# Performance work log

Measured on AMD Instinct MI355X. Metric: run time of the kernel, lower is better.

The kernel has to match this reference:

```python
import jax, jax.numpy as jnp
import numpy as np

D_MODEL = 768
N_HEADS = 12


def setup_inputs() -> dict:
    key = jax.random.key(0)
    ks = jax.random.split(key, 9)
    s = 1.0 / np.sqrt(D_MODEL)
    return {
        "x": jax.random.normal(ks[0], (1, 4096, D_MODEL), dtype=jnp.float32),
        "w_q": jax.random.normal(ks[1], (D_MODEL, D_MODEL), dtype=jnp.float32) * s,
        "b_q": jnp.zeros((D_MODEL,), dtype=jnp.float32),
        "w_k": jax.random.normal(ks[2], (D_MODEL, D_MODEL), dtype=jnp.float32) * s,
        "b_k": jnp.zeros((D_MODEL,), dtype=jnp.float32),
        "w_v": jax.random.normal(ks[3], (D_MODEL, D_MODEL), dtype=jnp.float32) * s,
        "b_v": jnp.zeros((D_MODEL,), dtype=jnp.float32),
        "w_o": jax.random.normal(ks[4], (D_MODEL, D_MODEL), dtype=jnp.float32) * s,
        "b_o": jnp.zeros((D_MODEL,), dtype=jnp.float32),
    }


def reference(x, w_q, b_q, w_k, b_k, w_v, b_v, w_o, b_o):
    b, l, dm = x.shape
    h = N_HEADS
    dk = dm // h
    # projections ([b,l,dm] @ [dm,dm]) then split heads -> [b,h,l,dk]
    def proj(w, bias):
        y = x @ w + bias
        return y.reshape(b, l, h, dk).transpose(0, 2, 1, 3)
    q = proj(w_q, b_q)
    k = proj(w_k, b_k)
    v = proj(w_v, b_v)
    scale = jnp.asarray(dk, x.dtype) ** 0.5
    scores = jnp.einsum("bhqd,bhkd->bhqk", q, k)  # [b,h,l,l]
    causal = jnp.triu(jnp.ones((l, l), dtype=bool), k=1)
    scores = jnp.where(causal, -jnp.inf, scores)
    weights = jax.nn.softmax(scores / scale, axis=-1)
    heads = jnp.einsum("bhqk,bhkd->bhqd", weights, v)  # [b,h,l,dk]
    heads = heads.transpose(0, 2, 1, 3).reshape(b, l, dm)
    return heads @ w_o + b_o
```

## Files before the change

kernel.cpp:

```cpp
#include <hip/hip_runtime.h>

#define L_SEQ 4096
#define DMODEL 768
#define NH 12
#define DK 64

typedef __bf16 bf16;
typedef __bf16 bf16x8 __attribute__((ext_vector_type(8)));
typedef __bf16 bf16x4 __attribute__((ext_vector_type(4)));
typedef float f32x4 __attribute__((ext_vector_type(4)));

#define QSCALE 0.1803368801111204f
#define DEFER_THR 8.0f

__device__ __forceinline__ void gload16(const void* g, void* l) {
    __builtin_amdgcn_global_load_lds(
        (const __attribute__((address_space(1))) unsigned int*)g,
        (__attribute__((address_space(3))) unsigned int*)l, 16, 0, 0);
}

__global__ __launch_bounds__(256) void prep_kernel(
    const float* __restrict__ x,
    const float* __restrict__ w_q, const float* __restrict__ w_k,
    const float* __restrict__ w_v, const float* __restrict__ w_o,
    bf16* __restrict__ xb, bf16* __restrict__ wqt, bf16* __restrict__ wkt,
    bf16* __restrict__ wvt, bf16* __restrict__ wot)
{
    const int bid = blockIdx.x;
    const int t = threadIdx.x;
    if (bid < 576) {
        __shared__ bf16 Ls[64][72];
        const int mat = bid / 144;
        const int tile = bid % 144;
        const int k0 = (tile / 12) * 64;
        const int c0 = (tile % 12) * 64;
        const float* W = mat == 0 ? w_q : mat == 1 ? w_k : mat == 2 ? w_v : w_o;
        bf16* WT = mat == 0 ? wqt : mat == 1 ? wkt : mat == 2 ? wvt : wot;
        #pragma unroll
        for (int p = 0; p < 4; ++p) {
            int id = t + p * 256;
            int r = id >> 4, c4 = id & 15;
            float4 v = *(const float4*)(W + (size_t)(k0 + r) * DMODEL + c0 + c4 * 4);
            bf16x4 b; b[0] = (bf16)v.x; b[1] = (bf16)v.y; b[2] = (bf16)v.z; b[3] = (bf16)v.w;
            *(bf16x4*)&Ls[r][c4 * 4] = b;
        }
        __syncthreads();
        #pragma unroll
        for (int p = 0; p < 2; ++p) {
            int id = t + p * 256;
            int crow = id >> 3, kc = id & 7;
            bf16x8 o;
            #pragma unroll
            for (int e = 0; e < 8; ++e) o[e] = Ls[kc * 8 + e][crow];
            *(bf16x8*)(WT + (size_t)(c0 + crow) * DMODEL + k0 + kc * 8) = o;
        }
    } else {
        const size_t base = (size_t)(bid - 576) * 4096;
        #pragma unroll
        for (int p = 0; p < 4; ++p) {
            size_t idx = base + (size_t)(t + p * 256) * 4;
            float4 v = *(const float4*)(x + idx);
            bf16x4 b; b[0] = (bf16)v.x; b[1] = (bf16)v.y; b[2] = (bf16)v.z; b[3] = (bf16)v.w;
            *(bf16x4*)(xb + idx) = b;
        }
    }
}

__global__ __launch_bounds__(256) void proj_kernel(
    const bf16* __restrict__ xb,
    const bf16* __restrict__ wqt, const bf16* __restrict__ wkt, const bf16* __restrict__ wvt,
    const float* __restrict__ b_q, const float* __restrict__ b_k, const float* __restrict__ b_v,
    bf16* __restrict__ qbuf, bf16* __restrict__ kbuf, bf16* __restrict__ vt)
{
    __shared__ bf16 As[128][72];
    __shared__ bf16 Bs[64][72];
    const int t = threadIdx.x;
    const int w = t >> 6, l = t & 63;
    const int lg = l >> 4, lr = l & 15;

    if (blockIdx.x < 768) {
        const int bn = blockIdx.x % 24;
        const int bm = blockIdx.x / 24;
        const int m0 = bm * 128;
        const int gn0 = bn * 64;
        const int sel = gn0 / DMODEL;
        const int c0 = gn0 % DMODEL;
        const bf16* WT = sel ? wkt : wqt;
        const float* bias = sel ? b_k : b_q;
        const float scale = sel ? 1.0f : QSCALE;

        f32x4 acc[2][4];
        #pragma unroll
        for (int i = 0; i < 2; i++)
            #pragma unroll
            for (int j = 0; j < 4; j++) acc[i][j] = (f32x4){0.f, 0.f, 0.f, 0.f};

        for (int kk = 0; kk < DMODEL; kk += 64) {
            #pragma unroll
            for (int p = 0; p < 4; ++p) {
                int id = t + p * 256;
                int row = id >> 3, ch = id & 7;
                *(bf16x8*)&As[row][ch * 8] =
                    *(const bf16x8*)(xb + (size_t)(m0 + row) * DMODEL + kk + ch * 8);
            }
            #pragma unroll
            for (int p = 0; p < 2; ++p) {
                int id = t + p * 256;
                int n = id >> 3, ch = id & 7;
                *(bf16x8*)&Bs[n][ch * 8] =
                    *(const bf16x8*)(WT + (size_t)(c0 + n) * DMODEL + kk + ch * 8);
            }
            __syncthreads();
            #pragma unroll
            for (int ks = 0; ks < 2; ++ks) {
                bf16x8 a[2], bfr[4];
                #pragma unroll
                for (int i = 0; i < 2; i++) a[i] = *(const bf16x8*)&As[w * 32 + i * 16 + lr][ks * 32 + lg * 8];
                #pragma unroll
                for (int j = 0; j < 4; j++) bfr[j] = *(const bf16x8*)&Bs[j * 16 + lr][ks * 32 + lg * 8];
                #pragma unroll
                for (int i = 0; i < 2; i++)
                    #pragma unroll
                    for (int j = 0; j < 4; j++)
                        acc[i][j] = __builtin_amdgcn_mfma_f32_16x16x32_bf16(a[i], bfr[j], acc[i][j], 0, 0, 0);
            }
            __syncthreads();
        }
        #pragma unroll
        for (int i = 0; i < 2; i++) {
            #pragma unroll
            for (int j = 0; j < 4; j++) {
                int c = c0 + j * 16 + lr;
                int h = c >> 6, d = c & 63;
                float bb = bias[c];
                #pragma unroll
                for (int r = 0; r < 4; r++) {
                    int m = m0 + w * 32 + i * 16 + lg * 4 + r;
                    float v = (acc[i][j][r] + bb) * scale;
                    if (sel == 0) {
                        qbuf[((size_t)h * L_SEQ + m) * DK + d] = (bf16)v;
                    } else {
                        size_t idx = (size_t)h * L_SEQ * DK + (size_t)(m >> 6) * 4096
                                   + (size_t)(m & 63) * 64 + (((d >> 3) ^ (m & 7)) << 3) + (d & 7);
                        kbuf[idx] = (bf16)v;
                    }
                }
            }
        }
    } else {
        const int bid = blockIdx.x - 768;
        const int bc = bid % 12;
        const int bmm = bid / 12;
        const int c0 = bc * 64;
        const int mm0 = bmm * 128;

        f32x4 acc[8];
        #pragma unroll
        for (int j = 0; j < 8; j++) acc[j] = (f32x4){0.f, 0.f, 0.f, 0.f};

        for (int kk = 0; kk < DMODEL; kk += 64) {
            #pragma unroll
            for (int p = 0; p < 4; ++p) {
                int id = t + p * 256;
                int row = id >> 3, ch = id & 7;
                *(bf16x8*)&As[row][ch * 8] =
                    *(const bf16x8*)(xb + (size_t)(mm0 + row) * DMODEL + kk + ch * 8);
            }
            #pragma unroll
            for (int p = 0; p < 2; ++p) {
                int id = t + p * 256;
                int n = id >> 3, ch = id & 7;
                *(bf16x8*)&Bs[n][ch * 8] =
                    *(const bf16x8*)(wvt + (size_t)(c0 + n) * DMODEL + kk + ch * 8);
            }
            __syncthreads();
            #pragma unroll
            for (int ks = 0; ks < 2; ++ks) {
                bf16x8 a = *(const bf16x8*)&Bs[w * 16 + lr][ks * 32 + lg * 8];
                #pragma unroll
                for (int j = 0; j < 8; j++) {
                    bf16x8 b = *(const bf16x8*)&As[j * 16 + lr][ks * 32 + lg * 8];
                    acc[j] = __builtin_amdgcn_mfma_f32_16x16x32_bf16(a, b, acc[j], 0, 0, 0);
                }
            }
            __syncthreads();
        }
        #pragma unroll
        for (int j = 0; j < 8; j++) {
            int m = mm0 + j * 16 + lr;
            #pragma unroll
            for (int r = 0; r < 4; r++) {
                int c = c0 + w * 16 + lg * 4 + r;
                float v = acc[j][r] + b_v[c];
                size_t idx = (size_t)(c >> 6) * DK * L_SEQ + (size_t)(m >> 6) * 4096
                           + (size_t)(c & 63) * 64 + ((((m >> 3) & 7) ^ (c & 7)) << 3) + (m & 7);
                vt[idx] = (bf16)v;
            }
        }
    }
}

__global__ __launch_bounds__(512) void attn_kernel(
    const bf16* __restrict__ qbuf, const bf16* __restrict__ kbuf,
    const bf16* __restrict__ vt, bf16* __restrict__ obuf)
{
    __shared__ __align__(16) char lds[65536];

    const int bid = blockIdx.x;
    const int h  = bid % NH;
    const int qt = 63 - (bid / NH);
    const int q0 = qt * 64;
    const int nt = qt + 1;
    const int nit = (nt + 1) >> 1;

    const int t = threadIdx.x;
    const int w = t >> 6;
    const int g = w >> 2;
    const int wg = w & 3;
    const int l = t & 63;
    const int lg = l >> 4, lr = l & 15;
    const int tg = t & 255;
    const int sw = (lr & 7) << 4;

    float* mergeAcc = (float*)lds;
    float* mergeM   = (float*)(lds + 22528);

    const size_t qrow = (size_t)h * L_SEQ + q0 + wg * 16 + lr;
    const bf16x8 qa0 = *(const bf16x8*)(qbuf + qrow * DK + 0  + lg * 8);
    const bf16x8 qa1 = *(const bf16x8*)(qbuf + qrow * DK + 32 + lg * 8);

    bf16x8 ones;
    #pragma unroll
    for (int e = 0; e < 8; ++e) ones[e] = (bf16)1.0f;

    f32x4 acc[4];
    #pragma unroll
    for (int j = 0; j < 4; j++) acc[j] = (f32x4){0.f, 0.f, 0.f, 0.f};
    f32x4 acc_sum = (f32x4){0.f, 0.f, 0.f, 0.f};
    float run_m = -1e30f;

    const bf16* kb_base = kbuf + (size_t)h * L_SEQ * DK;
    const bf16* vt_base = vt + (size_t)h * DK * L_SEQ;

    if (g < nt) {
        const bf16* kg = kb_base + (size_t)g * 4096;
        const bf16* vg = vt_base + (size_t)g * 4096;
        char* kl = lds + (size_t)(g << 1) * 8192;
        char* vl = lds + 32768 + (size_t)(g << 1) * 8192;
        #pragma unroll
        for (int p = 0; p < 2; ++p) {
            int id = tg + p * 256;
            gload16(kg + id * 8, kl + id * 16);
            gload16(vg + id * 8, vl + id * 16);
        }
    }

    for (int it = 0; it < nit; ++it) {
        const int cur = 2 * it + g;
        const bool active = (cur < nt);
        const int b = it & 1;
        asm volatile("s_waitcnt vmcnt(0)" ::: "memory");
        __builtin_amdgcn_sched_barrier(0);
        __builtin_amdgcn_s_barrier();
        const int nxt = cur + 2;
        if (nxt < nt) {
            const bf16* kg = kb_base + (size_t)nxt * 4096;
            const bf16* vg = vt_base + (size_t)nxt * 4096;
            char* kl = lds + (size_t)((g << 1) | (b ^ 1)) * 8192;
            char* vl = lds + 32768 + (size_t)((g << 1) | (b ^ 1)) * 8192;
            #pragma unroll
            for (int p = 0; p < 2; ++p) {
                int id = tg + p * 256;
                gload16(kg + id * 8, kl + id * 16);
                gload16(vg + id * 8, vl + id * 16);
            }
        }
        if (active) {
            char* Kbase = lds + (size_t)((g << 1) | b) * 8192;
            char* Vbase = lds + 32768 + (size_t)((g << 1) | b) * 8192;
            f32x4 s[4];
            #pragma unroll
            for (int j = 0; j < 4; j++) s[j] = (f32x4){0.f, 0.f, 0.f, 0.f};
            __builtin_amdgcn_s_setprio(1);
            #pragma unroll
            for (int dh = 0; dh < 2; ++dh) {
                const bf16x8 qa = dh ? qa1 : qa0;
                #pragma unroll
                for (int j = 0; j < 4; j++) {
                    bf16x8 kb = *(const bf16x8*)(Kbase + (j * 16 + lr) * 128 + ((dh * 64 + lg * 16) ^ sw));
                    s[j] = __builtin_amdgcn_mfma_f32_16x16x32_bf16(kb, qa, s[j], 0, 0, 0);
                }
            }
            __builtin_amdgcn_s_setprio(0);
            if (cur == qt) {
                const int qoff = wg * 16 + lr;
                #pragma unroll
                for (int j = 0; j < 4; j++)
                    #pragma unroll
                    for (int r = 0; r < 4; r++)
                        if (j * 16 + lg * 4 + r > qoff) s[j][r] = -3e30f;
            }
            float m0 = fmaxf(fmaxf(s[0][0], s[0][1]), s[0][2]);
            float m1 = fmaxf(fmaxf(s[0][3], s[1][0]), s[1][1]);
            float m2 = fmaxf(fmaxf(s[1][2], s[1][3]), s[2][0]);
            float m3 = fmaxf(fmaxf(s[2][1], s[2][2]), s[2][3]);
            float m4 = fmaxf(fmaxf(s[3][0], s[3][1]), s[3][2]);
            float t1 = fmaxf(fmaxf(m0, m1), m2);
            float t2 = fmaxf(fmaxf(m3, m4), s[3][3]);
            float mx = fmaxf(t1, t2);
            mx = fmaxf(mx, __shfl_xor(mx, 16));
            mx = fmaxf(mx, __shfl_xor(mx, 32));
            if (!__all(mx <= run_m + DEFER_THR)) {
                const float nm = fmaxf(run_m, mx);
                const float scq = exp2f(run_m - nm);
                run_m = nm;
                float sc0 = __shfl(scq, lg * 4 + 0);
                float sc1 = __shfl(scq, lg * 4 + 1);
                float sc2 = __shfl(scq, lg * 4 + 2);
                float sc3 = __shfl(scq, lg * 4 + 3);
                #pragma unroll
                for (int jd = 0; jd < 4; jd++) {
                    acc[jd][0] *= sc0; acc[jd][1] *= sc1;
                    acc[jd][2] *= sc2; acc[jd][3] *= sc3;
                }
                acc_sum[0] *= sc0; acc_sum[1] *= sc1;
                acc_sum[2] *= sc2; acc_sum[3] *= sc3;
            }
            unsigned Wp[4][2];
            #pragma unroll
            for (int j = 0; j < 4; j++) {
                float e0 = exp2f(s[j][0] - run_m);
                float e1 = exp2f(s[j][1] - run_m);
                float e2 = exp2f(s[j][2] - run_m);
                float e3 = exp2f(s[j][3] - run_m);
                asm("v_cvt_pk_bf16_f32 %0, %1, %2" : "=v"(Wp[j][0]) : "v"(e0), "v"(e1));
                asm("v_cvt_pk_bf16_f32 %0, %1, %2" : "=v"(Wp[j][1]) : "v"(e2), "v"(e3));
            }
            __builtin_amdgcn_s_setprio(1);
            #pragma unroll
            for (int dh = 0; dh < 2; ++dh) {
                unsigned x0 = Wp[2 * dh][0], y0 = Wp[2 * dh + 1][0];
                unsigned x1 = Wp[2 * dh][1], y1 = Wp[2 * dh + 1][1];
                asm("v_permlane32_swap_b32 %0, %1" : "+v"(x0), "+v"(y0));
                asm("v_permlane16_swap_b32 %0, %1" : "+v"(x0), "+v"(y0));
                asm("v_permlane32_swap_b32 %0, %1" : "+v"(x1), "+v"(y1));
                asm("v_permlane16_swap_b32 %0, %1" : "+v"(x1), "+v"(y1));
                union { unsigned u[4]; bf16x8 v; } pk;
                pk.u[0] = x0; pk.u[1] = x1; pk.u[2] = y0; pk.u[3] = y1;
                const bf16x8 pa = pk.v;
                acc_sum = __builtin_amdgcn_mfma_f32_16x16x32_bf16(pa, ones, acc_sum, 0, 0, 0);
                #pragma unroll
                for (int jd = 0; jd < 4; jd++) {
                    bf16x8 vb = *(const bf16x8*)(Vbase + (jd * 16 + lr) * 128 + ((dh * 64 + lg * 16) ^ sw));
                    acc[jd] = __builtin_amdgcn_mfma_f32_16x16x32_bf16(pa, vb, acc[jd], 0, 0, 0);
                }
            }
            __builtin_amdgcn_s_setprio(0);
        }
    }

    __syncthreads();
    if (g == 1) {
        float* base = mergeAcc + (size_t)(wg * 64 + l) * 21;
        #pragma unroll
        for (int jd = 0; jd < 4; jd++)
            #pragma unroll
            for (int r = 0; r < 4; r++) base[jd * 4 + r] = acc[jd][r];
        #pragma unroll
        for (int r = 0; r < 4; r++) base[16 + r] = acc_sum[r];
        mergeM[wg * 64 + l] = run_m;
    }
    __syncthreads();
    if (g == 0) {
        const float* base = mergeAcc + (size_t)(wg * 64 + l) * 21;
        const float mB = mergeM[wg * 64 + l];
        const float mF = fmaxf(run_m, mB);
        const float sa = exp2f(run_m - mF);
        const float sb = exp2f(mB - mF);
        float a4[4], b4[4];
        #pragma unroll
        for (int r = 0; r < 4; r++) {
            a4[r] = __shfl(sa, lg * 4 + r);
            b4[r] = __shfl(sb, lg * 4 + r);
        }
        #pragma unroll
        for (int jd = 0; jd < 4; jd++) {
            #pragma unroll
            for (int r = 0; r < 4; r++) {
                float denom = acc_sum[r] * a4[r] + base[16 + r] * b4[r];
                float v = acc[jd][r] * a4[r] + base[jd * 4 + r] * b4[r];
                int m = q0 + wg * 16 + lg * 4 + r;
                obuf[(size_t)m * DMODEL + h * DK + jd * 16 + lr] = (bf16)(v / denom);
            }
        }
    }
}

__global__ __launch_bounds__(256) void out_proj_kernel(
    const bf16* __restrict__ obuf, const bf16* __restrict__ wot,
    const float* __restrict__ b_o, float* __restrict__ out)
{
    __shared__ bf16 As[128][72];
    __shared__ bf16 Bts[64][72];
    const int bn = blockIdx.x % 12;
    const int bm = blockIdx.x / 12;
    const int m0 = bm * 128, c0 = bn * 64;
    const int t = threadIdx.x;
    const int w = t >> 6, l = t & 63, lg = l >> 4, lr = l & 15;

    f32x4 acc[2][4];
    #pragma unroll
    for (int i = 0; i < 2; i++)
        #pragma unroll
        for (int j = 0; j < 4; j++) acc[i][j] = (f32x4){0.f, 0.f, 0.f, 0.f};

    for (int kk = 0; kk < DMODEL; kk += 64) {
        #pragma unroll
        for (int p = 0; p < 4; ++p) {
            int id = t + p * 256;
            int row = id >> 3, ch = id & 7;
            *(bf16x8*)&As[row][ch * 8] =
                *(const bf16x8*)(obuf + (size_t)(m0 + row) * DMODEL + kk + ch * 8);
        }
        #pragma unroll
        for (int p = 0; p < 2; ++p) {
            int id = t + p * 256;
            int n = id >> 3, ch = id & 7;
            *(bf16x8*)&Bts[n][ch * 8] =
                *(const bf16x8*)(wot + (size_t)(c0 + n) * DMODEL + kk + ch * 8);
        }
        __syncthreads();
        #pragma unroll
        for (int ks = 0; ks < 2; ++ks) {
            bf16x8 a[2], bfr[4];
            #pragma unroll
            for (int i = 0; i < 2; i++) a[i] = *(const bf16x8*)&As[w * 32 + i * 16 + lr][ks * 32 + lg * 8];
            #pragma unroll
            for (int j = 0; j < 4; j++) bfr[j] = *(const bf16x8*)&Bts[j * 16 + lr][ks * 32 + lg * 8];
            #pragma unroll
            for (int i = 0; i < 2; i++)
                #pragma unroll
                for (int j = 0; j < 4; j++)
                    acc[i][j] = __builtin_amdgcn_mfma_f32_16x16x32_bf16(a[i], bfr[j], acc[i][j], 0, 0, 0);
        }
        __syncthreads();
    }
    #pragma unroll
    for (int i = 0; i < 2; i++) {
        #pragma unroll
        for (int j = 0; j < 4; j++) {
            int c = c0 + j * 16 + lr;
            float bb = b_o[c];
            #pragma unroll
            for (int r = 0; r < 4; r++) {
                int m = m0 + w * 32 + i * 16 + lg * 4 + r;
                out[(size_t)m * DMODEL + c] = acc[i][j][r] + bb;
            }
        }
    }
}

extern "C" void kernel_launch(void* const* d_in, const int* in_sizes, int n_in,
                              void* d_out, int out_size, void* d_ws, size_t ws_size,
                              hipStream_t stream) {
    const float* x   = (const float*)d_in[0];
    const float* w_q = (const float*)d_in[1];
    const float* b_q = (const float*)d_in[2];
    const float* w_k = (const float*)d_in[3];
    const float* b_k = (const float*)d_in[4];
    const float* w_v = (const float*)d_in[5];
    const float* b_v = (const float*)d_in[6];
    const float* w_o = (const float*)d_in[7];
    const float* b_o = (const float*)d_in[8];
    float* out = (float*)d_out;

    char* ws = (char*)d_ws;
    const size_t SZ = (size_t)NH * L_SEQ * DK * sizeof(bf16);
    const size_t WTSZ = (size_t)DMODEL * DMODEL * sizeof(bf16);
    bf16* qbuf = (bf16*)(ws);
    bf16* kbuf = (bf16*)(ws + SZ);
    bf16* vt   = (bf16*)(ws + 2 * SZ);
    bf16* obuf = (bf16*)(ws + 3 * SZ);
    bf16* xb   = (bf16*)(ws + 4 * SZ);
    bf16* wqt  = (bf16*)(ws + 5 * SZ);
    bf16* wkt  = (bf16*)(ws + 5 * SZ + WTSZ);
    bf16* wvt  = (bf16*)(ws + 5 * SZ + 2 * WTSZ);
    bf16* wot  = (bf16*)(ws + 5 * SZ + 3 * WTSZ);

    prep_kernel<<<dim3(1344), dim3(256), 0, stream>>>(x, w_q, w_k, w_v, w_o, xb, wqt, wkt, wvt, wot);
    proj_kernel<<<dim3(1152), dim3(256), 0, stream>>>(xb, wqt, wkt, wvt, b_q, b_k, b_v, qbuf, kbuf, vt);
    attn_kernel<<<dim3(768), dim3(512), 0, stream>>>(qbuf, kbuf, vt, obuf);
    out_proj_kernel<<<dim3(384), dim3(256), 0, stream>>>(obuf, wot, b_o, out);
}
```

Measured before the change: 115.3 us.

## Unify QKV projection into one 128x128-tiled GEMM with direct global-to-LDS loads

Packs the transposed Q/K/V weights into one concatenated buffer so a single GEMM with 128x128 tiles (2x2 waves, 4x4 MFMA fragments each) computes all three projections. The output projection gets the same tile shape. Both GEMMs now load through global_load_lds straight into unpadded LDS, with no register staging. Larger tiles raise data reuse and halve block counts, but they also drop LDS padding, which can cause bank conflicts on fragment reads. The out-projection grid falls to 192 blocks, which may underfill the GPU.

```diff
diff --git a/kernel.cpp b/kernel.cpp
--- a/kernel.cpp
+++ b/kernel.cpp
@@ -23,8 +23,7 @@
     const float* __restrict__ x,
     const float* __restrict__ w_q, const float* __restrict__ w_k,
     const float* __restrict__ w_v, const float* __restrict__ w_o,
-    bf16* __restrict__ xb, bf16* __restrict__ wqt, bf16* __restrict__ wkt,
-    bf16* __restrict__ wvt, bf16* __restrict__ wot)
+    bf16* __restrict__ xb, bf16* __restrict__ wcat, bf16* __restrict__ wot)
 {
     const int bid = blockIdx.x;
     const int t = threadIdx.x;
@@ -35,7 +34,8 @@
         const int k0 = (tile / 12) * 64;
         const int c0 = (tile % 12) * 64;
         const float* W = mat == 0 ? w_q : mat == 1 ? w_k : mat == 2 ? w_v : w_o;
-        bf16* WT = mat == 0 ? wqt : mat == 1 ? wkt : mat == 2 ? wvt : wot;
+        bf16* WT = (mat == 3) ? wot : wcat;
+        const int nbase = (mat == 3) ? 0 : mat * DMODEL;
         #pragma unroll
         for (int p = 0; p < 4; ++p) {
             int id = t + p * 256;
@@ -52,7 +52,7 @@
             bf16x8 o;
             #pragma unroll
             for (int e = 0; e < 8; ++e) o[e] = Ls[kc * 8 + e][crow];
-            *(bf16x8*)(WT + (size_t)(c0 + crow) * DMODEL + k0 + kc * 8) = o;
+            *(bf16x8*)(WT + (size_t)(nbase + c0 + crow) * DMODEL + k0 + kc * 8) = o;
         }
     } else {
         const size_t base = (size_t)(bid - 576) * 4096;
@@ -66,135 +66,78 @@
     }
 }
 
-__global__ __launch_bounds__(256) void proj_kernel(
-    const bf16* __restrict__ xb,
-    const bf16* __restrict__ wqt, const bf16* __restrict__ wkt, const bf16* __restrict__ wvt,
+__global__ __launch_bounds__(256) void qkv_gemm_kernel(
+    const bf16* __restrict__ xb, const bf16* __restrict__ wcat,
     const float* __restrict__ b_q, const float* __restrict__ b_k, const float* __restrict__ b_v,
     bf16* __restrict__ qbuf, bf16* __restrict__ kbuf, bf16* __restrict__ vt)
 {
-    __shared__ bf16 As[128][72];
-    __shared__ bf16 Bs[64][72];
+    __shared__ __align__(16) bf16 As[128][64];
+    __shared__ __align__(16) bf16 Bs[128][64];
+    const int bn = blockIdx.x % 18;
+    const int bm = blockIdx.x / 18;
+    const int m0 = bm * 128, gn0 = bn * 128;
     const int t = threadIdx.x;
     const int w = t >> 6, l = t & 63;
     const int lg = l >> 4, lr = l & 15;
-
-    if (blockIdx.x < 768) {
-        const int bn = blockIdx.x % 24;
-        const int bm = blockIdx.x / 24;
-        const int m0 = bm * 128;
-        const int gn0 = bn * 64;
-        const int sel = gn0 / DMODEL;
-        const int c0 = gn0 % DMODEL;
-        const bf16* WT = sel ? wkt : wqt;
-        const float* bias = sel ? b_k : b_q;
-        const float scale = sel ? 1.0f : QSCALE;
-
-        f32x4 acc[2][4];
-        #pragma unroll
-        for (int i = 0; i < 2; i++)
-            #pragma unroll
-            for (int j = 0; j < 4; j++) acc[i][j] = (f32x4){0.f, 0.f, 0.f, 0.f};
-
-        for (int kk = 0; kk < DMODEL; kk += 64) {
-            #pragma unroll
-            for (int p = 0; p < 4; ++p) {
-                int id = t + p * 256;
-                int row = id >> 3, ch = id & 7;
-                *(bf16x8*)&As[row][ch * 8] =
-                    *(const bf16x8*)(xb + (size_t)(m0 + row) * DMODEL + kk + ch * 8);
-            }
-            #pragma unroll
-            for (int p = 0; p < 2; ++p) {
-                int id = t + p * 256;
-                int n = id >> 3, ch = id & 7;
-                *(bf16x8*)&Bs[n][ch * 8] =
-                    *(const bf16x8*)(WT + (size_t)(c0 + n) * DMODEL + kk + ch * 8);
-            }
-            __syncthreads();
-            #pragma unroll
-            for (int ks = 0; ks < 2; ++ks) {
-                bf16x8 a[2], bfr[4];
-                #pragma unroll
-                for (int i = 0; i < 2; i++) a[i] = *(const bf16x8*)&As[w * 32 + i * 16 + lr][ks * 32 + lg * 8];
-                #pragma unroll
-                for (int j = 0; j < 4; j++) bfr[j] = *(const bf16x8*)&Bs[j * 16 + lr][ks * 32 + lg * 8];
-                #pragma unroll
-                for (int i = 0; i < 2; i++)
-                    #pragma unroll
-                    for (int j = 0; j < 4; j++)
-                        acc[i][j] = __builtin_amdgcn_mfma_f32_16x16x32_bf16(a[i], bfr[j], acc[i][j], 0, 0, 0);
-            }
-            __syncthreads();
-        }
-        #pragma unroll
-        for (int i = 0; i < 2; i++) {
-            #pragma unroll
-            for (int j = 0; j < 4; j++) {
-                int c = c0 + j * 16 + lr;
-                int h = c >> 6, d = c & 63;
-                float bb = bias[c];
-                #pragma unroll
-                for (int r = 0; r < 4; r++) {
-                    int m = m0 + w * 32 + i * 16 + lg * 4 + r;
-                    float v = (acc[i][j][r] + bb) * scale;
-                    if (sel == 0) {
-                        qbuf[((size_t)h * L_SEQ + m) * DK + d] = (bf16)v;
-                    } else {
-                        size_t idx = (size_t)h * L_SEQ * DK + (size_t)(m >> 6) * 4096
-                                   + (size_t)(m & 63) * 64 + (((d >> 3) ^ (m & 7)) << 3) + (d & 7);
-                        kbuf[idx] = (bf16)v;
-                    }
+    const int wr = w >> 1, wc = w & 1;
+
+    f32x4 acc[4][4];
+    #pragma unroll
+    for (int i = 0; i < 4; i++)
+        #pragma unroll
+        for (int j = 0; j < 4; j++) acc[i][j] = (f32x4){0.f, 0.f, 0.f, 0.f};
+
+    for (int kk = 0; kk < DMODEL; kk += 64) {
+        #pragma unroll
+        for (int p = 0; p < 4; ++p) {
+            int id = t + p * 256;
+            int row = id >> 3, ch = id & 7;
+            gload16(xb + (size_t)(m0 + row) * DMODEL + kk + ch * 8, (char*)As + id * 16);
+            gload16(wcat + (size_t)(gn0 + row) * DMODEL + kk + ch * 8, (char*)Bs + id * 16);
+        }
+        __syncthreads();
+        #pragma unroll
+        for (int ks = 0; ks < 2; ++ks) {
+            bf16x8 af[4], bfr[4];
+            #pragma unroll
+            for (int i = 0; i < 4; i++) af[i] = *(const bf16x8*)&As[wr * 64 + i * 16 + lr][ks * 32 + lg * 8];
+            #pragma unroll
+            for (int j = 0; j < 4; j++) bfr[j] = *(const bf16x8*)&Bs[wc * 64 + j * 16 + lr][ks * 32 + lg * 8];
+            #pragma unroll
+            for (int i = 0; i < 4; i++)
+                #pragma unroll
+                for (int j = 0; j < 4; j++)
+                    acc[i][j] = __builtin_amdgcn_mfma_f32_16x16x32_bf16(af[i], bfr[j], acc[i][j], 0, 0, 0);
+        }
+        __syncthreads();
+    }
+
+    const int sel = bn / 6;
+    const float* bias = sel == 0 ? b_q : sel == 1 ? b_k : b_v;
+    const float scale = sel == 0 ? QSCALE : 1.0f;
+    const int cb = gn0 - sel * DMODEL + wc * 64;
+    #pragma unroll
+    for (int j = 0; j < 4; j++) {
+        const int c = cb + j * 16 + lr;
+        const int h = c >> 6, d = c & 63;
+        const float bb = bias[c];
+        #pragma unroll
+        for (int i = 0; i < 4; i++) {
+            #pragma unroll
+            for (int r = 0; r < 4; r++) {
+                const int m = m0 + wr * 64 + i * 16 + lg * 4 + r;
+                const float v = (acc[i][j][r] + bb) * scale;
+                if (sel == 0) {
+                    qbuf[((size_t)h * L_SEQ + m) * DK + d] = (bf16)v;
+                } else if (sel == 1) {
+                    size_t idx = (size_t)h * L_SEQ * DK + (size_t)(m >> 6) * 4096
+                               + (size_t)(m & 63) * 64 + (((d >> 3) ^ (m & 7)) << 3) + (d & 7);
+                    kbuf[idx] = (bf16)v;
+                } else {
+                    size_t idx = (size_t)h * DK * L_SEQ + (size_t)(m >> 6) * 4096
+                               + (size_t)d * 64 + ((((m >> 3) & 7) ^ (d & 7)) << 3) + (m & 7);
+                    vt[idx] = (bf16)v;
                 }
-            }
-        }
-    } else {
-        const int bid = blockIdx.x - 768;
-        const int bc = bid % 12;
-        const int bmm = bid / 12;
-        const int c0 = bc * 64;
-        const int mm0 = bmm * 128;
-
-        f32x4 acc[8];
-        #pragma unroll
-        for (int j = 0; j < 8; j++) acc[j] = (f32x4){0.f, 0.f, 0.f, 0.f};
-
-        for (int kk = 0; kk < DMODEL; kk += 64) {
-            #pragma unroll
-            for (int p = 0; p < 4; ++p) {
-                int id = t + p * 256;
-                int row = id >> 3, ch = id & 7;
-                *(bf16x8*)&As[row][ch * 8] =
-                    *(const bf16x8*)(xb + (size_t)(mm0 + row) * DMODEL + kk + ch * 8);
-            }
-            #pragma unroll
-            for (int p = 0; p < 2; ++p) {
-                int id = t + p * 256;
-                int n = id >> 3, ch = id & 7;
-                *(bf16x8*)&Bs[n][ch * 8] =
-                    *(const bf16x8*)(wvt + (size_t)(c0 + n) * DMODEL + kk + ch * 8);
-            }
-            __syncthreads();
-            #pragma unroll
-            for (int ks = 0; ks < 2; ++ks) {
-                bf16x8 a = *(const bf16x8*)&Bs[w * 16 + lr][ks * 32 + lg * 8];
-                #pragma unroll
-                for (int j = 0; j < 8; j++) {
-                    bf16x8 b = *(const bf16x8*)&As[j * 16 + lr][ks * 32 + lg * 8];
-                    acc[j] = __builtin_amdgcn_mfma_f32_16x16x32_bf16(a, b, acc[j], 0, 0, 0);
-                }
-            }
-            __syncthreads();
-        }
-        #pragma unroll
-        for (int j = 0; j < 8; j++) {
-            int m = mm0 + j * 16 + lr;
-            #pragma unroll
-            for (int r = 0; r < 4; r++) {
-                int c = c0 + w * 16 + lg * 4 + r;
-                float v = acc[j][r] + b_v[c];
-                size_t idx = (size_t)(c >> 6) * DK * L_SEQ + (size_t)(m >> 6) * 4096
-                           + (size_t)(c & 63) * 64 + ((((m >> 3) & 7) ^ (c & 7)) << 3) + (m & 7);
-                vt[idx] = (bf16)v;
             }
         }
     }
@@ -396,21 +339,23 @@
     }
 }
 
-__global__ __launch_bounds__(256) void out_proj_kernel(
+__global__ __launch_bounds__(256) void out_gemm_kernel(
     const bf16* __restrict__ obuf, const bf16* __restrict__ wot,
     const float* __restrict__ b_o, float* __restrict__ out)
 {
-    __shared__ bf16 As[128][72];
-    __shared__ bf16 Bts[64][72];
-    const int bn = blockIdx.x % 12;
-    const int bm = blockIdx.x / 12;
-    const int m0 = bm * 128, c0 = bn * 64;
+    __shared__ __align__(16) bf16 As[128][64];
+    __shared__ __align__(16) bf16 Bs[128][64];
+    const int bn = blockIdx.x % 6;
+    const int bm = blockIdx.x / 6;
+    const int m0 = bm * 128, gn0 = bn * 128;
     const int t = threadIdx.x;
-    const int w = t >> 6, l = t & 63, lg = l >> 4, lr = l & 15;
-
-    f32x4 acc[2][4];
-    #pragma unroll
-    for (int i = 0; i < 2; i++)
+    const int w = t >> 6, l = t & 63;
+    const int lg = l >> 4, lr = l & 15;
+    const int wr = w >> 1, wc = w & 1;
+
+    f32x4 acc[4][4];
+    #pragma unroll
+    for (int i = 0; i < 4; i++)
         #pragma unroll
         for (int j = 0; j < 4; j++) acc[i][j] = (f32x4){0.f, 0.f, 0.f, 0.f};
 
@@ -419,41 +364,35 @@
         for (int p = 0; p < 4; ++p) {
             int id = t + p * 256;
             int row = id >> 3, ch = id & 7;
-            *(bf16x8*)&As[row][ch * 8] =
-                *(const bf16x8*)(obuf + (size_t)(m0 + row) * DMODEL + kk + ch * 8);
-        }
-        #pragma unroll
-        for (int p = 0; p < 2; ++p) {
-            int id = t + p * 256;
-            int n = id >> 3, ch = id & 7;
-            *(bf16x8*)&Bts[n][ch * 8] =
-                *(const bf16x8*)(wot + (size_t)(c0 + n) * DMODEL + kk + ch * 8);
+            gload16(obuf + (size_t)(m0 + row) * DMODEL + kk + ch * 8, (char*)As + id * 16);
+            gload16(wot + (size_t)(gn0 + row) * DMODEL + kk + ch * 8, (char*)Bs + id * 16);
         }
         __syncthreads();
         #pragma unroll
         for (int ks = 0; ks < 2; ++ks) {
-            bf16x8 a[2], bfr[4];
-            #pragma unroll
-            for (int i = 0; i < 2; i++) a[i] = *(const bf16x8*)&As[w * 32 + i * 16 + lr][ks * 32 + lg * 8];
-            #pragma unroll
-            for (int j = 0; j < 4; j++) bfr[j] = *(const bf16x8*)&Bts[j * 16 + lr][ks * 32 + lg * 8];
-            #pragma unroll
-            for (int i = 0; i < 2; i++)
+            bf16x8 af[4], bfr[4];
+            #pragma unroll
+            for (int i = 0; i < 4; i++) af[i] = *(const bf16x8*)&As[wr * 64 + i * 16 + lr][ks * 32 + lg * 8];
+            #pragma unroll
+            for (int j = 0; j < 4; j++) bfr[j] = *(const bf16x8*)&Bs[wc * 64 + j * 16 + lr][ks * 32 + lg * 8];
+            #pragma unroll
+            for (int i = 0; i < 4; i++)
                 #pragma unroll
                 for (int j = 0; j < 4; j++)
-                    acc[i][j] = __builtin_amdgcn_mfma_f32_16x16x32_bf16(a[i], bfr[j], acc[i][j], 0, 0, 0);
+                    acc[i][j] = __builtin_amdgcn_mfma_f32_16x16x32_bf16(af[i], bfr[j], acc[i][j], 0, 0, 0);
         }
         __syncthreads();
     }
-    #pragma unroll
-    for (int i = 0; i < 2; i++) {
-        #pragma unroll
-        for (int j = 0; j < 4; j++) {
-            int c = c0 + j * 16 + lr;
-            float bb = b_o[c];
+
+    #pragma unroll
+    for (int j = 0; j < 4; j++) {
+        const int c = gn0 + wc * 64 + j * 16 + lr;
+        const float bb = b_o[c];
+        #pragma unroll
+        for (int i = 0; i < 4; i++) {
             #pragma unroll
             for (int r = 0; r < 4; r++) {
-                int m = m0 + w * 32 + i * 16 + lg * 4 + r;
+                const int m = m0 + wr * 64 + i * 16 + lg * 4 + r;
                 out[(size_t)m * DMODEL + c] = acc[i][j][r] + bb;
             }
         }
@@ -482,13 +421,11 @@
     bf16* vt   = (bf16*)(ws + 2 * SZ);
     bf16* obuf = (bf16*)(ws + 3 * SZ);
     bf16* xb   = (bf16*)(ws + 4 * SZ);
-    bf16* wqt  = (bf16*)(ws + 5 * SZ);
-    bf16* wkt  = (bf16*)(ws + 5 * SZ + WTSZ);
-    bf16* wvt  = (bf16*)(ws + 5 * SZ + 2 * WTSZ);
+    bf16* wcat = (bf16*)(ws + 5 * SZ);
     bf16* wot  = (bf16*)(ws + 5 * SZ + 3 * WTSZ);
 
-    prep_kernel<<<dim3(1344), dim3(256), 0, stream>>>(x, w_q, w_k, w_v, w_o, xb, wqt, wkt, wvt, wot);
-    proj_kernel<<<dim3(1152), dim3(256), 0, stream>>>(xb, wqt, wkt, wvt, b_q, b_k, b_v, qbuf, kbuf, vt);
+    prep_kernel<<<dim3(1344), dim3(256), 0, stream>>>(x, w_q, w_k, w_v, w_o, xb, wcat, wot);
+    qkv_gemm_kernel<<<dim3(576), dim3(256), 0, stream>>>(xb, wcat, b_q, b_k, b_v, qbuf, kbuf, vt);
     attn_kernel<<<dim3(768), dim3(512), 0, stream>>>(qbuf, kbuf, vt, obuf);
-    out_proj_kernel<<<dim3(384), dim3(256), 0, stream>>>(obuf, wot, b_o, out);
-}
+    out_gemm_kernel<<<dim3(192), dim3(256), 0, stream>>>(obuf, wot, b_o, out);
+}
```

After: 134.5 us. +16.7%, slower.

## Split longest causal query tiles across two blocks with atomic-flag merge

Applied to the files above, without the earlier changes.

The 16 longest query tiles per head (qt 48-63) are split into two blocks that each process half of the KV range. Partial outputs, row sums and maxima go to a global scratch buffer, and whichever block finishes second merges them using an atomic counter. The goal is to reduce tail imbalance in the causal workload across the grid. The cost is an extra memset launch, more blocks, global partial traffic and fences. Partials reuse the xb workspace region, which prep and proj have already consumed by this point.

```diff
diff --git a/kernel.cpp b/kernel.cpp
--- a/kernel.cpp
+++ b/kernel.cpp
@@ -202,16 +202,33 @@
 
 __global__ __launch_bounds__(512) void attn_kernel(
     const bf16* __restrict__ qbuf, const bf16* __restrict__ kbuf,
-    const bf16* __restrict__ vt, bf16* __restrict__ obuf)
+    const bf16* __restrict__ vt, bf16* __restrict__ obuf,
+    float* __restrict__ partial, int* __restrict__ flags)
 {
     __shared__ __align__(16) char lds[65536];
 
     const int bid = blockIdx.x;
-    const int h  = bid % NH;
-    const int qt = 63 - (bid / NH);
+    int h, qt, kvt0, ntL, si = -1, half = 0;
+    if (bid < 192) {
+        h = bid % NH; qt = 47 - bid / NH;
+        kvt0 = 0; ntL = qt + 1;
+    } else if (bid < 576) {
+        int sid = bid - 192;
+        half = sid / 192;
+        int r2 = sid % 192;
+        h = r2 % NH; qt = 63 - r2 / NH;
+        si = (63 - qt) * NH + h;
+        int nt = qt + 1, n0 = nt >> 1;
+        kvt0 = half ? n0 : 0;
+        ntL = half ? (nt - n0) : n0;
+    } else {
+        int rid = bid - 576;
+        h = rid % NH; qt = 31 - rid / NH;
+        kvt0 = 0; ntL = qt + 1;
+    }
     const int q0 = qt * 64;
-    const int nt = qt + 1;
-    const int nit = (nt + 1) >> 1;
+    const int nit = (ntL + 1) >> 1;
+    const bool isSplit = (si >= 0);
 
     const int t = threadIdx.x;
     const int w = t >> 6;
@@ -224,6 +241,7 @@
 
     float* mergeAcc = (float*)lds;
     float* mergeM   = (float*)(lds + 22528);
+    int* ldsFlag    = (int*)(lds + 23552);
 
     const size_t qrow = (size_t)h * L_SEQ + q0 + wg * 16 + lr;
     const bf16x8 qa0 = *(const bf16x8*)(qbuf + qrow * DK + 0  + lg * 8);
@@ -242,9 +260,9 @@
     const bf16* kb_base = kbuf + (size_t)h * L_SEQ * DK;
     const bf16* vt_base = vt + (size_t)h * DK * L_SEQ;
 
-    if (g < nt) {
-        const bf16* kg = kb_base + (size_t)g * 4096;
-        const bf16* vg = vt_base + (size_t)g * 4096;
+    if (g < ntL) {
+        const bf16* kg = kb_base + (size_t)(kvt0 + g) * 4096;
+        const bf16* vg = vt_base + (size_t)(kvt0 + g) * 4096;
         char* kl = lds + (size_t)(g << 1) * 8192;
         char* vl = lds + 32768 + (size_t)(g << 1) * 8192;
         #pragma unroll
@@ -256,16 +274,17 @@
     }
 
     for (int it = 0; it < nit; ++it) {
-        const int cur = 2 * it + g;
-        const bool active = (cur < nt);
+        const int curl = 2 * it + g;
+        const bool active = (curl < ntL);
+        const int gt = kvt0 + curl;
         const int b = it & 1;
         asm volatile("s_waitcnt vmcnt(0)" ::: "memory");
         __builtin_amdgcn_sched_barrier(0);
         __builtin_amdgcn_s_barrier();
-        const int nxt = cur + 2;
-        if (nxt < nt) {
-            const bf16* kg = kb_base + (size_t)nxt * 4096;
-            const bf16* vg = vt_base + (size_t)nxt * 4096;
+        const int nxtl = curl + 2;
+        if (nxtl < ntL) {
+            const bf16* kg = kb_base + (size_t)(kvt0 + nxtl) * 4096;
+            const bf16* vg = vt_base + (size_t)(kvt0 + nxtl) * 4096;
             char* kl = lds + (size_t)((g << 1) | (b ^ 1)) * 8192;
             char* vl = lds + 32768 + (size_t)((g << 1) | (b ^ 1)) * 8192;
             #pragma unroll
@@ -292,7 +311,7 @@
                 }
             }
             __builtin_amdgcn_s_setprio(0);
-            if (cur == qt) {
+            if (gt == qt) {
                 const int qoff = wg * 16 + lr;
                 #pragma unroll
                 for (int j = 0; j < 4; j++)
@@ -371,6 +390,7 @@
         mergeM[wg * 64 + l] = run_m;
     }
     __syncthreads();
+    float vout[4][4], denom4[4], mrow[4];
     if (g == 0) {
         const float* base = mergeAcc + (size_t)(wg * 64 + l) * 21;
         const float mB = mergeM[wg * 64 + l];
@@ -382,15 +402,61 @@
         for (int r = 0; r < 4; r++) {
             a4[r] = __shfl(sa, lg * 4 + r);
             b4[r] = __shfl(sb, lg * 4 + r);
-        }
-        #pragma unroll
-        for (int jd = 0; jd < 4; jd++) {
+            mrow[r] = __shfl(mF, lg * 4 + r);
+        }
+        #pragma unroll
+        for (int r = 0; r < 4; r++)
+            denom4[r] = acc_sum[r] * a4[r] + base[16 + r] * b4[r];
+        #pragma unroll
+        for (int jd = 0; jd < 4; jd++)
+            #pragma unroll
+            for (int r = 0; r < 4; r++)
+                vout[jd][r] = acc[jd][r] * a4[r] + base[jd * 4 + r] * b4[r];
+        if (!isSplit) {
+            #pragma unroll
+            for (int jd = 0; jd < 4; jd++)
+                #pragma unroll
+                for (int r = 0; r < 4; r++) {
+                    int m = q0 + wg * 16 + lg * 4 + r;
+                    obuf[(size_t)m * DMODEL + h * DK + jd * 16 + lr] = (bf16)(vout[jd][r] / denom4[r]);
+                }
+        } else {
+            float* prow = partial + (size_t)(si * 2 + half) * 64 * 66;
             #pragma unroll
             for (int r = 0; r < 4; r++) {
-                float denom = acc_sum[r] * a4[r] + base[16 + r] * b4[r];
-                float v = acc[jd][r] * a4[r] + base[jd * 4 + r] * b4[r];
-                int m = q0 + wg * 16 + lg * 4 + r;
-                obuf[(size_t)m * DMODEL + h * DK + jd * 16 + lr] = (bf16)(v / denom);
+                const int row = wg * 16 + lg * 4 + r;
+                #pragma unroll
+                for (int jd = 0; jd < 4; jd++)
+                    prow[row * 66 + jd * 16 + lr] = vout[jd][r];
+                if (lr == 0) prow[row * 66 + 64] = denom4[r];
+                if (lr == 1) prow[row * 66 + 65] = mrow[r];
+            }
+        }
+    }
+
+    if (isSplit) {
+        __threadfence();
+        __syncthreads();
+        if (t == 0) *ldsFlag = atomicAdd(&flags[si], 1);
+        __syncthreads();
+        if (*ldsFlag == 1 && g == 0) {
+            __threadfence();
+            const float* orow = partial + (size_t)(si * 2 + (half ^ 1)) * 64 * 66;
+            #pragma unroll
+            for (int r = 0; r < 4; r++) {
+                const int row = wg * 16 + lg * 4 + r;
+                const float sO = orow[row * 66 + 64];
+                const float mO = orow[row * 66 + 65];
+                const float M = fmaxf(mrow[r], mO);
+                const float al = exp2f(mrow[r] - M);
+                const float be = exp2f(mO - M);
+                const float den = denom4[r] * al + sO * be;
+                const int m = q0 + row;
+                #pragma unroll
+                for (int jd = 0; jd < 4; jd++) {
+                    float vm = vout[jd][r] * al + orow[row * 66 + jd * 16 + lr] * be;
+                    obuf[(size_t)m * DMODEL + h * DK + jd * 16 + lr] = (bf16)(vm / den);
+                }
             }
         }
     }
@@ -486,9 +552,12 @@
     bf16* wkt  = (bf16*)(ws + 5 * SZ + WTSZ);
     bf16* wvt  = (bf16*)(ws + 5 * SZ + 2 * WTSZ);
     bf16* wot  = (bf16*)(ws + 5 * SZ + 3 * WTSZ);
+    float* partial = (float*)(ws + 4 * SZ);
+    int*   flags   = (int*)(ws + 4 * SZ + 7 * 1024 * 1024);
 
     prep_kernel<<<dim3(1344), dim3(256), 0, stream>>>(x, w_q, w_k, w_v, w_o, xb, wqt, wkt, wvt, wot);
     proj_kernel<<<dim3(1152), dim3(256), 0, stream>>>(xb, wqt, wkt, wvt, b_q, b_k, b_v, qbuf, kbuf, vt);
-    attn_kernel<<<dim3(768), dim3(512), 0, stream>>>(qbuf, kbuf, vt, obuf);
+    hipMemsetAsync(flags, 0, 192 * sizeof(int), stream);
+    attn_kernel<<<dim3(960), dim3(512), 0, stream>>>(qbuf, kbuf, vt, obuf, partial, flags);
     out_proj_kernel<<<dim3(384), dim3(256), 0, stream>>>(obuf, wot, b_o, out);
 }
```

Result: slower. 227.1 us (+96.9%).

## Restructure attention: 128-row query tiles per block, drop split-KV merge

Applied to the files above, without the earlier changes.

Attention blocks previously handled 64 query rows with two wave groups splitting the KV tiles and merging partial softmax state through LDS. Now each 512-thread block covers 128 query rows, one per 16-row wave, and all eight waves stream the same K/V tiles, halving the grid and LDS use. This reuses each loaded K/V tile across twice as many queries and removes the merge step and its barriers. In exchange the serial KV loop per block is twice as long, with 384 blocks on the GPU, and the work per block is less balanced.

```diff
diff --git a/kernel.cpp b/kernel.cpp
--- a/kernel.cpp
+++ b/kernel.cpp
@@ -204,28 +204,21 @@
     const bf16* __restrict__ qbuf, const bf16* __restrict__ kbuf,
     const bf16* __restrict__ vt, bf16* __restrict__ obuf)
 {
-    __shared__ __align__(16) char lds[65536];
+    __shared__ __align__(16) char lds[32768];
 
     const int bid = blockIdx.x;
     const int h  = bid % NH;
-    const int qt = 63 - (bid / NH);
-    const int q0 = qt * 64;
-    const int nt = qt + 1;
-    const int nit = (nt + 1) >> 1;
+    const int qt = 31 - bid / NH;
+    const int q0 = qt * 128;
+    const int nt = 2 * (qt + 1);
 
     const int t = threadIdx.x;
     const int w = t >> 6;
-    const int g = w >> 2;
-    const int wg = w & 3;
     const int l = t & 63;
     const int lg = l >> 4, lr = l & 15;
-    const int tg = t & 255;
     const int sw = (lr & 7) << 4;
 
-    float* mergeAcc = (float*)lds;
-    float* mergeM   = (float*)(lds + 22528);
-
-    const size_t qrow = (size_t)h * L_SEQ + q0 + wg * 16 + lr;
+    const size_t qrow = (size_t)h * L_SEQ + q0 + w * 16 + lr;
     const bf16x8 qa0 = *(const bf16x8*)(qbuf + qrow * DK + 0  + lg * 8);
     const bf16x8 qa1 = *(const bf16x8*)(qbuf + qrow * DK + 32 + lg * 8);
 
@@ -242,156 +235,111 @@
     const bf16* kb_base = kbuf + (size_t)h * L_SEQ * DK;
     const bf16* vt_base = vt + (size_t)h * DK * L_SEQ;
 
-    if (g < nt) {
-        const bf16* kg = kb_base + (size_t)g * 4096;
-        const bf16* vg = vt_base + (size_t)g * 4096;
-        char* kl = lds + (size_t)(g << 1) * 8192;
-        char* vl = lds + 32768 + (size_t)(g << 1) * 8192;
-        #pragma unroll
-        for (int p = 0; p < 2; ++p) {
-            int id = tg + p * 256;
-            gload16(kg + id * 8, kl + id * 16);
-            gload16(vg + id * 8, vl + id * 16);
-        }
-    }
-
-    for (int it = 0; it < nit; ++it) {
-        const int cur = 2 * it + g;
-        const bool active = (cur < nt);
+    gload16(kb_base + t * 8, lds + t * 16);
+    gload16(vt_base + t * 8, lds + 16384 + t * 16);
+
+    for (int it = 0; it < nt; ++it) {
         const int b = it & 1;
         asm volatile("s_waitcnt vmcnt(0)" ::: "memory");
         __builtin_amdgcn_sched_barrier(0);
         __builtin_amdgcn_s_barrier();
-        const int nxt = cur + 2;
-        if (nxt < nt) {
-            const bf16* kg = kb_base + (size_t)nxt * 4096;
-            const bf16* vg = vt_base + (size_t)nxt * 4096;
-            char* kl = lds + (size_t)((g << 1) | (b ^ 1)) * 8192;
-            char* vl = lds + 32768 + (size_t)((g << 1) | (b ^ 1)) * 8192;
-            #pragma unroll
-            for (int p = 0; p < 2; ++p) {
-                int id = tg + p * 256;
-                gload16(kg + id * 8, kl + id * 16);
-                gload16(vg + id * 8, vl + id * 16);
-            }
-        }
-        if (active) {
-            char* Kbase = lds + (size_t)((g << 1) | b) * 8192;
-            char* Vbase = lds + 32768 + (size_t)((g << 1) | b) * 8192;
-            f32x4 s[4];
-            #pragma unroll
-            for (int j = 0; j < 4; j++) s[j] = (f32x4){0.f, 0.f, 0.f, 0.f};
-            __builtin_amdgcn_s_setprio(1);
-            #pragma unroll
-            for (int dh = 0; dh < 2; ++dh) {
-                const bf16x8 qa = dh ? qa1 : qa0;
-                #pragma unroll
-                for (int j = 0; j < 4; j++) {
-                    bf16x8 kb = *(const bf16x8*)(Kbase + (j * 16 + lr) * 128 + ((dh * 64 + lg * 16) ^ sw));
-                    s[j] = __builtin_amdgcn_mfma_f32_16x16x32_bf16(kb, qa, s[j], 0, 0, 0);
-                }
-            }
-            __builtin_amdgcn_s_setprio(0);
-            if (cur == qt) {
-                const int qoff = wg * 16 + lr;
-                #pragma unroll
-                for (int j = 0; j < 4; j++)
-                    #pragma unroll
-                    for (int r = 0; r < 4; r++)
-                        if (j * 16 + lg * 4 + r > qoff) s[j][r] = -3e30f;
-            }
-            float m0 = fmaxf(fmaxf(s[0][0], s[0][1]), s[0][2]);
-            float m1 = fmaxf(fmaxf(s[0][3], s[1][0]), s[1][1]);
-            float m2 = fmaxf(fmaxf(s[1][2], s[1][3]), s[2][0]);
-            float m3 = fmaxf(fmaxf(s[2][1], s[2][2]), s[2][3]);
-            float m4 = fmaxf(fmaxf(s[3][0], s[3][1]), s[3][2]);
-            float t1 = fmaxf(fmaxf(m0, m1), m2);
-            float t2 = fmaxf(fmaxf(m3, m4), s[3][3]);
-            float mx = fmaxf(t1, t2);
-            mx = fmaxf(mx, __shfl_xor(mx, 16));
-            mx = fmaxf(mx, __shfl_xor(mx, 32));
-            if (!__all(mx <= run_m + DEFER_THR)) {
-                const float nm = fmaxf(run_m, mx);
-                const float scq = exp2f(run_m - nm);
-                run_m = nm;
-                float sc0 = __shfl(scq, lg * 4 + 0);
-                float sc1 = __shfl(scq, lg * 4 + 1);
-                float sc2 = __shfl(scq, lg * 4 + 2);
-                float sc3 = __shfl(scq, lg * 4 + 3);
-                #pragma unroll
-                for (int jd = 0; jd < 4; jd++) {
-                    acc[jd][0] *= sc0; acc[jd][1] *= sc1;
-                    acc[jd][2] *= sc2; acc[jd][3] *= sc3;
-                }
-                acc_sum[0] *= sc0; acc_sum[1] *= sc1;
-                acc_sum[2] *= sc2; acc_sum[3] *= sc3;
-            }
-            unsigned Wp[4][2];
+        if (it + 1 < nt) {
+            const bf16* kg = kb_base + (size_t)(it + 1) * 4096;
+            const bf16* vg = vt_base + (size_t)(it + 1) * 4096;
+            char* kl = lds + (size_t)(b ^ 1) * 8192;
+            char* vl = lds + 16384 + (size_t)(b ^ 1) * 8192;
+            gload16(kg + t * 8, kl + t * 16);
+            gload16(vg + t * 8, vl + t * 16);
+        }
+        char* Kbase = lds + (size_t)b * 8192;
+        char* Vbase = lds + 16384 + (size_t)b * 8192;
+        f32x4 s[4];
+        #pragma unroll
+        for (int j = 0; j < 4; j++) s[j] = (f32x4){0.f, 0.f, 0.f, 0.f};
+        __builtin_amdgcn_s_setprio(1);
+        #pragma unroll
+        for (int dh = 0; dh < 2; ++dh) {
+            const bf16x8 qa = dh ? qa1 : qa0;
             #pragma unroll
             for (int j = 0; j < 4; j++) {
-                float e0 = exp2f(s[j][0] - run_m);
-                float e1 = exp2f(s[j][1] - run_m);
-                float e2 = exp2f(s[j][2] - run_m);
-                float e3 = exp2f(s[j][3] - run_m);
-                asm("v_cvt_pk_bf16_f32 %0, %1, %2" : "=v"(Wp[j][0]) : "v"(e0), "v"(e1));
-                asm("v_cvt_pk_bf16_f32 %0, %1, %2" : "=v"(Wp[j][1]) : "v"(e2), "v"(e3));
-            }
-            __builtin_amdgcn_s_setprio(1);
-            #pragma unroll
-            for (int dh = 0; dh < 2; ++dh) {
-                unsigned x0 = Wp[2 * dh][0], y0 = Wp[2 * dh + 1][0];
-                unsigned x1 = Wp[2 * dh][1], y1 = Wp[2 * dh + 1][1];
-                asm("v_permlane32_swap_b32 %0, %1" : "+v"(x0), "+v"(y0));
-                asm("v_permlane16_swap_b32 %0, %1" : "+v"(x0), "+v"(y0));
-                asm("v_permlane32_swap_b32 %0, %1" : "+v"(x1), "+v"(y1));
-                asm("v_permlane16_swap_b32 %0, %1" : "+v"(x1), "+v"(y1));
-                union { unsigned u[4]; bf16x8 v; } pk;
-                pk.u[0] = x0; pk.u[1] = x1; pk.u[2] = y0; pk.u[3] = y1;
-                const bf16x8 pa = pk.v;
-                acc_sum = __builtin_amdgcn_mfma_f32_16x16x32_bf16(pa, ones, acc_sum, 0, 0, 0);
-                #pragma unroll
-                for (int jd = 0; jd < 4; jd++) {
-                    bf16x8 vb = *(const bf16x8*)(Vbase + (jd * 16 + lr) * 128 + ((dh * 64 + lg * 16) ^ sw));
-                    acc[jd] = __builtin_amdgcn_mfma_f32_16x16x32_bf16(pa, vb, acc[jd], 0, 0, 0);
-                }
-            }
-            __builtin_amdgcn_s_setprio(0);
-        }
-    }
-
-    __syncthreads();
-    if (g == 1) {
-        float* base = mergeAcc + (size_t)(wg * 64 + l) * 21;
-        #pragma unroll
-        for (int jd = 0; jd < 4; jd++)
-            #pragma unroll
-            for (int r = 0; r < 4; r++) base[jd * 4 + r] = acc[jd][r];
-        #pragma unroll
-        for (int r = 0; r < 4; r++) base[16 + r] = acc_sum[r];
-        mergeM[wg * 64 + l] = run_m;
-    }
-    __syncthreads();
-    if (g == 0) {
-        const float* base = mergeAcc + (size_t)(wg * 64 + l) * 21;
-        const float mB = mergeM[wg * 64 + l];
-        const float mF = fmaxf(run_m, mB);
-        const float sa = exp2f(run_m - mF);
-        const float sb = exp2f(mB - mF);
-        float a4[4], b4[4];
+                bf16x8 kb = *(const bf16x8*)(Kbase + (j * 16 + lr) * 128 + ((dh * 64 + lg * 16) ^ sw));
+                s[j] = __builtin_amdgcn_mfma_f32_16x16x32_bf16(kb, qa, s[j], 0, 0, 0);
+            }
+        }
+        __builtin_amdgcn_s_setprio(0);
+        if (it >= nt - 2) {
+            const int kvrel = (it - (nt - 2)) * 64;
+            const int qoff = w * 16 + lr;
+            #pragma unroll
+            for (int j = 0; j < 4; j++)
+                #pragma unroll
+                for (int r = 0; r < 4; r++)
+                    if (kvrel + j * 16 + lg * 4 + r > qoff) s[j][r] = -3e30f;
+        }
+        float m0 = fmaxf(fmaxf(s[0][0], s[0][1]), s[0][2]);
+        float m1 = fmaxf(fmaxf(s[0][3], s[1][0]), s[1][1]);
+        float m2 = fmaxf(fmaxf(s[1][2], s[1][3]), s[2][0]);
+        float m3 = fmaxf(fmaxf(s[2][1], s[2][2]), s[2][3]);
+        float m4 = fmaxf(fmaxf(s[3][0], s[3][1]), s[3][2]);
+        float t1 = fmaxf(fmaxf(m0, m1), m2);
+        float t2 = fmaxf(fmaxf(m3, m4), s[3][3]);
+        float mx = fmaxf(t1, t2);
+        mx = fmaxf(mx, __shfl_xor(mx, 16));
+        mx = fmaxf(mx, __shfl_xor(mx, 32));
+        if (!__all(mx <= run_m + DEFER_THR)) {
+            const float nm = fmaxf(run_m, mx);
+            const float scq = exp2f(run_m - nm);
+            run_m = nm;
+            float sc0 = __shfl(scq, lg * 4 + 0);
+            float sc1 = __shfl(scq, lg * 4 + 1);
+            float sc2 = __shfl(scq, lg * 4 + 2);
+            float sc3 = __shfl(scq, lg * 4 + 3);
+            #pragma unroll
+            for (int jd = 0; jd < 4; jd++) {
+                acc[jd][0] *= sc0; acc[jd][1] *= sc1;
+                acc[jd][2] *= sc2; acc[jd][3] *= sc3;
+            }
+            acc_sum[0] *= sc0; acc_sum[1] *= sc1;
+            acc_sum[2] *= sc2; acc_sum[3] *= sc3;
+        }
+        unsigned Wp[4][2];
+        #pragma unroll
+        for (int j = 0; j < 4; j++) {
+            float e0 = exp2f(s[j][0] - run_m);
+            float e1 = exp2f(s[j][1] - run_m);
+            float e2 = exp2f(s[j][2] - run_m);
+            float e3 = exp2f(s[j][3] - run_m);
+            asm("v_cvt_pk_bf16_f32 %0, %1, %2" : "=v"(Wp[j][0]) : "v"(e0), "v"(e1));
+            asm("v_cvt_pk_bf16_f32 %0, %1, %2" : "=v"(Wp[j][1]) : "v"(e2), "v"(e3));
+        }
+        __builtin_amdgcn_s_setprio(1);
+        #pragma unroll
+        for (int dh = 0; dh < 2; ++dh) {
+            unsigned x0 = Wp[2 * dh][0], y0 = Wp[2 * dh + 1][0];
+            unsigned x1 = Wp[2 * dh][1], y1 = Wp[2 * dh + 1][1];
+            asm("v_permlane32_swap_b32 %0, %1" : "+v"(x0), "+v"(y0));
+            asm("v_permlane16_swap_b32 %0, %1" : "+v"(x0), "+v"(y0));
+            asm("v_permlane32_swap_b32 %0, %1" : "+v"(x1), "+v"(y1));
+            asm("v_permlane16_swap_b32 %0, %1" : "+v"(x1), "+v"(y1));
+            union { unsigned u[4]; bf16x8 v; } pk;
+            pk.u[0] = x0; pk.u[1] = x1; pk.u[2] = y0; pk.u[3] = y1;
+            const bf16x8 pa = pk.v;
+            acc_sum = __builtin_amdgcn_mfma_f32_16x16x32_bf16(pa, ones, acc_sum, 0, 0, 0);
+            #pragma unroll
+            for (int jd = 0; jd < 4; jd++) {
+                bf16x8 vb = *(const bf16x8*)(Vbase + (jd * 16 + lr) * 128 + ((dh * 64 + lg * 16) ^ sw));
+                acc[jd] = __builtin_amdgcn_mfma_f32_16x16x32_bf16(pa, vb, acc[jd], 0, 0, 0);
+            }
+        }
+        __builtin_amdgcn_s_setprio(0);
+    }
+
+    #pragma unroll
+    for (int jd = 0; jd < 4; jd++) {
         #pragma unroll
         for (int r = 0; r < 4; r++) {
-            a4[r] = __shfl(sa, lg * 4 + r);
-            b4[r] = __shfl(sb, lg * 4 + r);
-        }
-        #pragma unroll
-        for (int jd = 0; jd < 4; jd++) {
-            #pragma unroll
-            for (int r = 0; r < 4; r++) {
-                float denom = acc_sum[r] * a4[r] + base[16 + r] * b4[r];
-                float v = acc[jd][r] * a4[r] + base[jd * 4 + r] * b4[r];
-                int m = q0 + wg * 16 + lg * 4 + r;
-                obuf[(size_t)m * DMODEL + h * DK + jd * 16 + lr] = (bf16)(v / denom);
-            }
+            int m = q0 + w * 16 + lg * 4 + r;
+            obuf[(size_t)m * DMODEL + h * DK + jd * 16 + lr] = (bf16)(acc[jd][r] / acc_sum[r]);
         }
     }
 }
@@ -489,6 +437,6 @@
 
     prep_kernel<<<dim3(1344), dim3(256), 0, stream>>>(x, w_q, w_k, w_v, w_o, xb, wqt, wkt, wvt, wot);
     proj_kernel<<<dim3(1152), dim3(256), 0, stream>>>(xb, wqt, wkt, wvt, b_q, b_k, b_v, qbuf, kbuf, vt);
-    attn_kernel<<<dim3(768), dim3(512), 0, stream>>>(qbuf, kbuf, vt, obuf);
+    attn_kernel<<<dim3(384), dim3(512), 0, stream>>>(qbuf, kbuf, vt, obuf);
     out_proj_kernel<<<dim3(384), dim3(256), 0, stream>>>(obuf, wot, b_o, out);
 }
```

Measured after the change: 134.6 us. +16.7%, slower.
